# Performance work log

Hardware: AMD Instinct MI355X
Metric: run time of the kernel (lower is better)

The kernel has to match this reference:

```python
import jax, jax.numpy as jnp
from jax import lax
import numpy as np

D_MODEL = 1024
D_STATE = 128
D_CONV = 4
EXPAND = 2
HEADDIM = 64
CHUNK = 10
D_INNER = EXPAND * D_MODEL          # 2048
NHEADS = D_INNER // HEADDIM         # 32
CONV_DIM = D_INNER + 2 * D_STATE    # 2304
BATCH, SEQ = 2, 1000


def setup_inputs() -> dict:
    key = jax.random.key(0)
    ks = jax.random.split(key, 9)
    n = lambda k, shp, sc: jax.random.normal(k, shp, dtype=jnp.float32) * sc
    return {
        "x": n(ks[0], (BATCH, SEQ, D_MODEL), 1.0),
        "W_in": n(ks[1], (2 * D_INNER + 2 * D_STATE + NHEADS, D_MODEL), 0.02),
        "conv_w": n(ks[2], (CONV_DIM, D_CONV), 0.2),
        "conv_b": n(ks[3], (CONV_DIM,), 0.02),
        "dt_bias": n(ks[4], (NHEADS,), 0.5),
        "A_log": jnp.log(jnp.linspace(1.0, 16.0, NHEADS)).astype(jnp.float32),
        "D": n(ks[6], (NHEADS,), 1.0),
        "norm_w": jnp.ones((D_INNER,), jnp.float32),
        "W_out": n(ks[8], (D_MODEL, D_INNER), 0.02),
    }


def segsum(x):
    # x: (..., T) -> (..., T, T) with out[i,j] = sum_{k=j+1..i} x_k for i>=j else -inf
    cs = jnp.cumsum(x, axis=-1)
    seg = cs[..., :, None] - cs[..., None, :]
    T = x.shape[-1]
    mask = jnp.tril(jnp.ones((T, T), bool))
    return jnp.where(mask, seg, -jnp.inf)


def ssd(x, A, Bm, Cm, chunk):
    # x: (b,l,h,p)  A: (b,l,h)  Bm,Cm: (b,l,n)  (ngroups=1, group dim squeezed)
    b, l, h, p = x.shape
    n = Bm.shape[-1]
    c = l // chunk
    xr = x.reshape(b, c, chunk, h, p)
    Ar = A.reshape(b, c, chunk, h).transpose(0, 3, 1, 2)      # (b,h,c,s)
    Br = Bm.reshape(b, c, chunk, n)
    Cr = Cm.reshape(b, c, chunk, n)
    Acs = jnp.cumsum(Ar, axis=-1)                              # (b,h,c,s)
    L = jnp.exp(segsum(Ar))                                    # (b,h,c,s,s)
    # intra-chunk (diagonal blocks)
    Y_diag = jnp.einsum('bcln,bcsn,bhcls,bcshp->bclhp', Cr, Br, L, xr)
    # per-chunk end states
    decay_states = jnp.exp(Acs[..., -1:] - Acs)                # (b,h,c,s)
    states = jnp.einsum('bcln,bhcl,bclhp->bchpn', Br, decay_states, xr)
    states = jnp.concatenate([jnp.zeros((b, 1, h, p, n), x.dtype), states], axis=1)
    # inter-chunk recurrence (parallel form)
    chunk_sums = jnp.pad(Acs[..., -1], ((0, 0), (0, 0), (1, 0)))  # (b,h,c+1)
    decay_chunk = jnp.exp(segsum(chunk_sums))                    # (b,h,c+1,c+1)
    new_states = jnp.einsum('bhzc,bchpn->bzhpn', decay_chunk, states)
    prev_states = new_states[:, :-1]                             # (b,c,h,p,n)
    # state -> output contribution
    Y_off = jnp.einsum('bcln,bchpn,bhcl->bclhp', Cr, prev_states, jnp.exp(Acs))
    return (Y_diag + Y_off).reshape(b, l, h, p)


def reference(x, W_in, conv_w, conv_b, dt_bias, A_log, D, norm_w, W_out):
    b, l, _ = x.shape
    zxbcdt = x @ W_in.T                                          # (b,l,4384)
    z = zxbcdt[..., :D_INNER]
    xBC = zxbcdt[..., D_INNER:D_INNER + CONV_DIM]
    dt = zxbcdt[..., D_INNER + CONV_DIM:]
    dt = jax.nn.softplus(dt + dt_bias)                           # (b,l,h)
    # causal depthwise conv1d
    xc = jnp.pad(xBC, ((0, 0), (D_CONV - 1, 0), (0, 0)))
    conv = lax.conv_general_dilated(
        xc.transpose(0, 2, 1), conv_w[:, None, :], (1,), 'VALID',
        feature_group_count=CONV_DIM,
        dimension_numbers=('NCH', 'OIH', 'NCH'))
    xBC = jax.nn.silu(conv.transpose(0, 2, 1) + conv_b)          # (b,l,conv_dim)
    x_ssm = xBC[..., :D_INNER].reshape(b, l, NHEADS, HEADDIM)
    Bm = xBC[..., D_INNER:D_INNER + D_STATE]
    Cm = xBC[..., D_INNER + D_STATE:]
    A = -jnp.exp(A_log)                                          # (h,)
    y = ssd(x_ssm * dt[..., None], A * dt, Bm, Cm, CHUNK)
    y = y + x_ssm * D[None, None, :, None]
    y = y.reshape(b, l, D_INNER)
    # gated RMSNorm
    y = y * jax.nn.silu(z)
    y = y * lax.rsqrt(jnp.mean(y * y, axis=-1, keepdims=True) + 1e-5) * norm_w
    return y @ W_out.T
```

## Files before the change

### kernel.cpp

```cpp
#include <hip/hip_runtime.h>
#include <hip/hip_bf16.h>

#define BATCHN 2
#define SEQL 1000
#define DMODEL 1024
#define DSTATE 128
#define HEADDIM 64
#define DINNER 2048
#define NHEADS 32
#define CONVDIM 2304
#define NPROJ 4384
#define TOKENS 2000
#define MPAD 2048
#define NPAD1 4480
#define QC 64
#define NCH 16

typedef __bf16 bfx8 __attribute__((ext_vector_type(8)));
typedef float fx4 __attribute__((ext_vector_type(4)));
typedef unsigned short u16x8 __attribute__((ext_vector_type(8)));

__device__ __forceinline__ unsigned short f2bf(float f) {
    unsigned int u = __builtin_bit_cast(unsigned int, f);
    u += 0x7FFFu + ((u >> 16) & 1u);
    return (unsigned short)(u >> 16);
}
__device__ __forceinline__ float bf2f(unsigned short u) {
    return __builtin_bit_cast(float, ((unsigned int)u) << 16);
}

__device__ __forceinline__ void gload16(const void* g, void* l) {
    __builtin_amdgcn_global_load_lds(
        (const __attribute__((address_space(1))) void*)g,
        (__attribute__((address_space(3))) void*)l, 16, 0, 0);
}

__global__ __launch_bounds__(256) void k_f2bf_pad(const float* __restrict__ src,
                                                  unsigned short* __restrict__ dst,
                                                  int n4src, int n4dst) {
    int i = blockIdx.x * 256 + threadIdx.x;
    if (i >= n4dst) return;
    ushort4 o = {0, 0, 0, 0};
    if (i < n4src) {
        float4 v = ((const float4*)src)[i];
        o.x = f2bf(v.x); o.y = f2bf(v.y); o.z = f2bf(v.z); o.w = f2bf(v.w);
    }
    ((ushort4*)dst)[i] = o;
}

__global__ __launch_bounds__(256) void k_dt(const float* __restrict__ x,
                                            const float* __restrict__ win,
                                            const float* __restrict__ dt_bias,
                                            float* __restrict__ dtv) {
    __shared__ float sx[8][1024];
    int t = threadIdx.x;
    int tok0 = blockIdx.x * 8;
    for (int i = t; i < 8 * 256; i += 256) {
        int tok = i >> 8, k4 = i & 255;
        ((float4*)&sx[tok][0])[k4] = ((const float4*)(x + (size_t)(tok0 + tok) * DMODEL))[k4];
    }
    __syncthreads();
    int tl = t >> 5, h = t & 31;
    const float4* wr_ = (const float4*)(win + (size_t)(2 * DINNER + 2 * DSTATE + h) * DMODEL);
    const float4* xr = (const float4*)&sx[tl][0];
    float acc = 0.f;
    #pragma unroll 4
    for (int k = 0; k < 256; ++k) {
        float4 a = xr[k], b = wr_[k];
        acc += a.x * b.x + a.y * b.y + a.z * b.z + a.w * b.w;
    }
    float v = acc + dt_bias[h];
    dtv[(size_t)(tok0 + tl) * NHEADS + h] = fmaxf(v, 0.f) + log1pf(expf(-fabsf(v)));
}

__global__ __launch_bounds__(256) void k_gemm64(const unsigned short* __restrict__ A,
                                                const unsigned short* __restrict__ B,
                                                float* __restrict__ C,
                                                int Mstore, int N, int K,
                                                int kc, size_t pstride) {
    __shared__ __attribute__((aligned(16))) unsigned short As[2][2048];
    __shared__ __attribute__((aligned(16))) unsigned short Bs[2][4096];
    int t = threadIdx.x;
    int lane = t & 63, wave = t >> 6;
    int wr = wave >> 1, wc = wave & 1;
    int m0 = blockIdx.y * 64, n0 = blockIdx.x * 128;
    int k0 = blockIdx.z * kc;
    int swcol = (((t & 3) ^ ((t >> 3) & 3)) * 8);
    const unsigned short* Ag = A + (size_t)(m0 + (t >> 2)) * K + k0 + swcol;
    const unsigned short* Bg = B + (size_t)(n0 + (t >> 2)) * K + k0 + swcol;
    int fr = lane & 15, ks = lane >> 4;
    int sl = (ks ^ ((fr >> 1) & 3)) << 3;
    fx4 acc[2][4] = {};
    gload16(Ag, &As[0][t * 8]);
    gload16(Bg, &Bs[0][t * 8]);
    gload16(Bg + (size_t)64 * K, &Bs[0][2048 + t * 8]);
    __syncthreads();
    int cur = 0;
    for (int kk = 32; kk < kc; kk += 32) {
        gload16(Ag + kk, &As[cur ^ 1][t * 8]);
        gload16(Bg + kk, &Bs[cur ^ 1][t * 8]);
        gload16(Bg + (size_t)64 * K + kk, &Bs[cur ^ 1][2048 + t * 8]);
        bfx8 a[2], b[4];
        #pragma unroll
        for (int m = 0; m < 2; ++m)
            a[m] = *(const bfx8*)&As[cur][(wr * 32 + m * 16 + fr) * 32 + sl];
        #pragma unroll
        for (int n = 0; n < 4; ++n)
            b[n] = *(const bfx8*)&Bs[cur][(wc * 64 + n * 16 + fr) * 32 + sl];
        #pragma unroll
        for (int m = 0; m < 2; ++m)
            #pragma unroll
            for (int n = 0; n < 4; ++n)
                acc[m][n] = __builtin_amdgcn_mfma_f32_16x16x32_bf16(a[m], b[n], acc[m][n], 0, 0, 0);
        __syncthreads();
        cur ^= 1;
    }
    {
        bfx8 a[2], b[4];
        #pragma unroll
        for (int m = 0; m < 2; ++m)
            a[m] = *(const bfx8*)&As[cur][(wr * 32 + m * 16 + fr) * 32 + sl];
        #pragma unroll
        for (int n = 0; n < 4; ++n)
            b[n] = *(const bfx8*)&Bs[cur][(wc * 64 + n * 16 + fr) * 32 + sl];
        #pragma unroll
        for (int m = 0; m < 2; ++m)
            #pragma unroll
            for (int n = 0; n < 4; ++n)
                acc[m][n] = __builtin_amdgcn_mfma_f32_16x16x32_bf16(a[m], b[n], acc[m][n], 0, 0, 0);
    }
    float* Cz = C + (size_t)blockIdx.z * pstride;
    #pragma unroll
    for (int m = 0; m < 2; ++m) {
        int rbase = m0 + wr * 32 + m * 16 + (lane >> 4) * 4;
        #pragma unroll
        for (int i = 0; i < 4; ++i) {
            int r = rbase + i;
            if (r < Mstore) {
                #pragma unroll
                for (int n = 0; n < 4; ++n) {
                    int c = n0 + wc * 64 + n * 16 + fr;
                    if (c < N) Cz[(size_t)r * N + c] = acc[m][n][i];
                }
            }
        }
    }
}

__global__ __launch_bounds__(256) void k_red(const float* __restrict__ part,
                                             float* __restrict__ out, int n4, size_t pstride4) {
    int i = blockIdx.x * 256 + threadIdx.x;
    if (i >= n4) return;
    const float4* p = (const float4*)part;
    float4 v0 = p[i];
    float4 v1 = p[i + pstride4];
    float4 v2 = p[i + 2 * pstride4];
    float4 v3 = p[i + 3 * pstride4];
    float4 o;
    o.x = (v0.x + v1.x) + (v2.x + v3.x);
    o.y = (v0.y + v1.y) + (v2.y + v3.y);
    o.z = (v0.z + v1.z) + (v2.z + v3.z);
    o.w = (v0.w + v1.w) + (v2.w + v3.w);
    ((float4*)out)[i] = o;
}

__global__ __launch_bounds__(256) void k_conv4(const float* __restrict__ zx,
                                               const float* __restrict__ cw,
                                               const float* __restrict__ cb,
                                               float* __restrict__ xbc) {
    int idx = blockIdx.x * 256 + threadIdx.x;
    if (idx >= (TOKENS / 4) * CONVDIM) return;
    int tg = idx / CONVDIM;
    int col = idx - tg * CONVDIM;
    int b = tg / 250;
    int l0 = (tg - b * 250) * 4;
    float in[7];
    #pragma unroll
    for (int j = 0; j < 7; ++j) {
        int lj = l0 - 3 + j;
        in[j] = (lj >= 0) ? zx[(size_t)(b * SEQL + lj) * NPROJ + DINNER + col] : 0.f;
    }
    float w0 = cw[col * 4], w1 = cw[col * 4 + 1], w2 = cw[col * 4 + 2], w3 = cw[col * 4 + 3];
    float bb = cb[col];
    #pragma unroll
    for (int i = 0; i < 4; ++i) {
        float a = bb + w0 * in[i] + w1 * in[i + 1] + w2 * in[i + 2] + w3 * in[i + 3];
        xbc[(size_t)(b * SEQL + l0 + i) * CONVDIM + col] = a / (1.f + expf(-a));
    }
}

#define SCW 136
#define SWW 72
__global__ __launch_bounds__(256) void k_tile(const float* __restrict__ xbc,
                                              const float* __restrict__ dtv,
                                              const float* __restrict__ A_log,
                                              const float* __restrict__ Dp,
                                              float* __restrict__ ybuf,
                                              float* __restrict__ Sg,
                                              float* __restrict__ cumA) {
    __shared__ unsigned short sC[64 * SCW];
    __shared__ unsigned short sB[64 * SCW];
    __shared__ unsigned short sBdT[128 * SWW];
    __shared__ unsigned short sXdT[64 * SWW];
    __shared__ unsigned short sXr[64 * SWW];
    __shared__ float sAcs[64];
    __shared__ float sdt[64];
    int bid = blockIdx.x;
    int b = bid / (NHEADS * NCH);
    int r = bid % (NHEADS * NCH);
    int h = r / NCH, c = r % NCH;
    int t = threadIdx.x;
    int lane = t & 63, wave = t >> 6;
    if (t < 64) {
        int tok = c * QC + t;
        float d = (tok < SEQL) ? dtv[(size_t)(b * SEQL + tok) * NHEADS + h] : 0.f;
        float A = -expf(A_log[h]);
        float v = A * d;
        #pragma unroll
        for (int off = 1; off < 64; off <<= 1) {
            float u = __shfl_up(v, off, 64);
            if (lane >= off) v += u;
        }
        sdt[t] = d;
        sAcs[t] = v;
        cumA[(size_t)bid * 64 + t] = v;
    }
    __syncthreads();
    float Aend = sAcs[63];
    for (int i = t; i < 64 * 32; i += 256) {
        int l = i >> 5, n4 = (i & 31) * 4;
        int tok = c * QC + l;
        float4 cv = {0, 0, 0, 0}, bv = {0, 0, 0, 0};
        if (tok < SEQL) {
            const float* base = xbc + (size_t)(b * SEQL + tok) * CONVDIM;
            bv = *(const float4*)(base + DINNER + n4);
            cv = *(const float4*)(base + DINNER + DSTATE + n4);
        }
        float dec = expf(Aend - sAcs[l]);
        sC[l * SCW + n4 + 0] = f2bf(cv.x); sC[l * SCW + n4 + 1] = f2bf(cv.y);
        sC[l * SCW + n4 + 2] = f2bf(cv.z); sC[l * SCW + n4 + 3] = f2bf(cv.w);
        sB[l * SCW + n4 + 0] = f2bf(bv.x); sB[l * SCW + n4 + 1] = f2bf(bv.y);
        sB[l * SCW + n4 + 2] = f2bf(bv.z); sB[l * SCW + n4 + 3] = f2bf(bv.w);
        sBdT[(n4 + 0) * SWW + l] = f2bf(bv.x * dec);
        sBdT[(n4 + 1) * SWW + l] = f2bf(bv.y * dec);
        sBdT[(n4 + 2) * SWW + l] = f2bf(bv.z * dec);
        sBdT[(n4 + 3) * SWW + l] = f2bf(bv.w * dec);
    }
    for (int i = t; i < 64 * 16; i += 256) {
        int l = i >> 4, p4 = (i & 15) * 4;
        int tok = c * QC + l;
        float4 xv = {0, 0, 0, 0};
        if (tok < SEQL) xv = *(const float4*)(xbc + (size_t)(b * SEQL + tok) * CONVDIM + h * 64 + p4);
        float d = sdt[l];
        sXr[l * SWW + p4 + 0] = f2bf(xv.x); sXr[l * SWW + p4 + 1] = f2bf(xv.y);
        sXr[l * SWW + p4 + 2] = f2bf(xv.z); sXr[l * SWW + p4 + 3] = f2bf(xv.w);
        sXdT[(p4 + 0) * SWW + l] = f2bf(xv.x * d);
        sXdT[(p4 + 1) * SWW + l] = f2bf(xv.y * d);
        sXdT[(p4 + 2) * SWW + l] = f2bf(xv.z * d);
        sXdT[(p4 + 3) * SWW + l] = f2bf(xv.w * d);
    }
    __syncthreads();
    int fr = lane & 15, fk8 = (lane >> 4) * 8;
    int wr = wave >> 1, wc = wave & 1;
    fx4 g[2][2] = {};
    #pragma unroll
    for (int k = 0; k < 4; ++k) {
        bfx8 a0 = *(const bfx8*)&sC[(wr * 32 + fr) * SCW + k * 32 + fk8];
        bfx8 a1 = *(const bfx8*)&sC[(wr * 32 + 16 + fr) * SCW + k * 32 + fk8];
        bfx8 b0 = *(const bfx8*)&sB[(wc * 32 + fr) * SCW + k * 32 + fk8];
        bfx8 b1 = *(const bfx8*)&sB[(wc * 32 + 16 + fr) * SCW + k * 32 + fk8];
        g[0][0] = __builtin_amdgcn_mfma_f32_16x16x32_bf16(a0, b0, g[0][0], 0, 0, 0);
        g[0][1] = __builtin_amdgcn_mfma_f32_16x16x32_bf16(a0, b1, g[0][1], 0, 0, 0);
        g[1][0] = __builtin_amdgcn_mfma_f32_16x16x32_bf16(a1, b0, g[1][0], 0, 0, 0);
        g[1][1] = __builtin_amdgcn_mfma_f32_16x16x32_bf16(a1, b1, g[1][1], 0, 0, 0);
    }
    __syncthreads();
    int rb = wr * 32 + (lane >> 4) * 4;
    int cb = wc * 32 + fr;
    #pragma unroll
    for (int m = 0; m < 2; ++m)
        #pragma unroll
        for (int n = 0; n < 2; ++n)
            #pragma unroll
            for (int i = 0; i < 4; ++i) {
                int row = rb + m * 16 + i, col = cb + n * 16;
                float wv = (col <= row) ? g[m][n][i] * expf(sAcs[row] - sAcs[col]) : 0.f;
                sB[row * SWW + col] = f2bf(wv);
            }
    __syncthreads();
    fx4 yd[2][2] = {};
    fx4 sc[2][4] = {};
    #pragma unroll
    for (int k = 0; k < 2; ++k) {
        bfx8 aW0 = *(const bfx8*)&sB[(wr * 32 + fr) * SWW + k * 32 + fk8];
        bfx8 aW1 = *(const bfx8*)&sB[(wr * 32 + 16 + fr) * SWW + k * 32 + fk8];
        bfx8 bX0 = *(const bfx8*)&sXdT[(wc * 32 + fr) * SWW + k * 32 + fk8];
        bfx8 bX1 = *(const bfx8*)&sXdT[(wc * 32 + 16 + fr) * SWW + k * 32 + fk8];
        yd[0][0] = __builtin_amdgcn_mfma_f32_16x16x32_bf16(aW0, bX0, yd[0][0], 0, 0, 0);
        yd[0][1] = __builtin_amdgcn_mfma_f32_16x16x32_bf16(aW0, bX1, yd[0][1], 0, 0, 0);
        yd[1][0] = __builtin_amdgcn_mfma_f32_16x16x32_bf16(aW1, bX0, yd[1][0], 0, 0, 0);
        yd[1][1] = __builtin_amdgcn_mfma_f32_16x16x32_bf16(aW1, bX1, yd[1][1], 0, 0, 0);
        bfx8 aX0 = *(const bfx8*)&sXdT[(wr * 32 + fr) * SWW + k * 32 + fk8];
        bfx8 aX1 = *(const bfx8*)&sXdT[(wr * 32 + 16 + fr) * SWW + k * 32 + fk8];
        #pragma unroll
        for (int j = 0; j < 4; ++j) {
            bfx8 bB = *(const bfx8*)&sBdT[(wc * 64 + j * 16 + fr) * SWW + k * 32 + fk8];
            sc[0][j] = __builtin_amdgcn_mfma_f32_16x16x32_bf16(aX0, bB, sc[0][j], 0, 0, 0);
            sc[1][j] = __builtin_amdgcn_mfma_f32_16x16x32_bf16(aX1, bB, sc[1][j], 0, 0, 0);
        }
    }
    float Dh = Dp[h];
    #pragma unroll
    for (int m = 0; m < 2; ++m)
        #pragma unroll
        for (int i = 0; i < 4; ++i) {
            int row = rb + m * 16 + i;
            int tok = c * QC + row;
            if (tok < SEQL) {
                #pragma unroll
                for (int n = 0; n < 2; ++n) {
                    int col = cb + n * 16;
                    float xr = bf2f(sXr[row * SWW + col]);
                    ybuf[(size_t)(b * SEQL + tok) * DINNER + h * 64 + col] = yd[m][n][i] + Dh * xr;
                }
            }
        }
    #pragma unroll
    for (int m = 0; m < 2; ++m)
        #pragma unroll
        for (int i = 0; i < 4; ++i) {
            int p = rb + m * 16 + i;
            #pragma unroll
            for (int j = 0; j < 4; ++j) {
                int n = wc * 64 + j * 16 + fr;
                Sg[(size_t)bid * 8192 + p * 128 + n] = sc[m][j][i];
            }
        }
}

__global__ __launch_bounds__(256) void k_scan2v(float* __restrict__ Sg,
                                                const float* __restrict__ cumA) {
    int bid = blockIdx.x;
    int bh = bid >> 5, sub = bid & 31;
    int e = sub * 256 + threadIdx.x;
    __shared__ float sT[NCH];
    if (threadIdx.x < NCH)
        sT[threadIdx.x] = cumA[((size_t)(bh * NCH) + threadIdx.x) * 64 + 63];
    __syncthreads();
    float S = 0.f;
    size_t base = (size_t)bh * NCH * 8192 + e;
    for (int g = 0; g < NCH; ++g) {
        size_t off = base + (size_t)g * 8192;
        float sg = Sg[off];
        Sg[off] = S;
        S = expf(sT[g]) * S + sg;
    }
}

__global__ __launch_bounds__(256) void k_yoff(const float* __restrict__ xbc,
                                              const float* __restrict__ Sg,
                                              const float* __restrict__ cumA,
                                              float* __restrict__ ybuf) {
    int bid = blockIdx.x;
    int b = bid / (NHEADS * NCH);
    int r = bid % (NHEADS * NCH);
    int h = r / NCH, c = r % NCH;
    if (c == 0) return;
    __shared__ unsigned short sC[64 * SCW];
    __shared__ unsigned short sS[64 * SCW];
    __shared__ float sE[64];
    int t = threadIdx.x;
    int lane = t & 63, wave = t >> 6;
    if (t < 64) sE[t] = expf(cumA[(size_t)bid * 64 + t]);
    for (int i = t; i < 64 * 32; i += 256) {
        int l = i >> 5, n4 = (i & 31) * 4;
        int tok = c * QC + l;
        float4 cv = {0, 0, 0, 0};
        if (tok < SEQL)
            cv = *(const float4*)(xbc + (size_t)(b * SEQL + tok) * CONVDIM + DINNER + DSTATE + n4);
        sC[l * SCW + n4 + 0] = f2bf(cv.x); sC[l * SCW + n4 + 1] = f2bf(cv.y);
        sC[l * SCW + n4 + 2] = f2bf(cv.z); sC[l * SCW + n4 + 3] = f2bf(cv.w);
        float4 sv = *(const float4*)(Sg + (size_t)bid * 8192 + l * 128 + n4);
        sS[l * SCW + n4 + 0] = f2bf(sv.x); sS[l * SCW + n4 + 1] = f2bf(sv.y);
        sS[l * SCW + n4 + 2] = f2bf(sv.z); sS[l * SCW + n4 + 3] = f2bf(sv.w);
    }
    __syncthreads();
    int fr = lane & 15, fk8 = (lane >> 4) * 8;
    int wr = wave >> 1, wc = wave & 1;
    fx4 yo[2][2] = {};
    #pragma unroll
    for (int k = 0; k < 4; ++k) {
        bfx8 a0 = *(const bfx8*)&sC[(wr * 32 + fr) * SCW + k * 32 + fk8];
        bfx8 a1 = *(const bfx8*)&sC[(wr * 32 + 16 + fr) * SCW + k * 32 + fk8];
        bfx8 b0 = *(const bfx8*)&sS[(wc * 32 + fr) * SCW + k * 32 + fk8];
        bfx8 b1 = *(const bfx8*)&sS[(wc * 32 + 16 + fr) * SCW + k * 32 + fk8];
        yo[0][0] = __builtin_amdgcn_mfma_f32_16x16x32_bf16(a0, b0, yo[0][0], 0, 0, 0);
        yo[0][1] = __builtin_amdgcn_mfma_f32_16x16x32_bf16(a0, b1, yo[0][1], 0, 0, 0);
        yo[1][0] = __builtin_amdgcn_mfma_f32_16x16x32_bf16(a1, b0, yo[1][0], 0, 0, 0);
        yo[1][1] = __builtin_amdgcn_mfma_f32_16x16x32_bf16(a1, b1, yo[1][1], 0, 0, 0);
    }
    int rb = wr * 32 + (lane >> 4) * 4;
    int cb = wc * 32 + fr;
    #pragma unroll
    for (int m = 0; m < 2; ++m)
        #pragma unroll
        for (int i = 0; i < 4; ++i) {
            int row = rb + m * 16 + i;
            int tok = c * QC + row;
            if (tok < SEQL) {
                float e = sE[row];
                #pragma unroll
                for (int n = 0; n < 2; ++n) {
                    int col = cb + n * 16;
                    size_t off = (size_t)(b * SEQL + tok) * DINNER + h * 64 + col;
                    ybuf[off] += yo[m][n][i] * e;
                }
            }
        }
}

__global__ __launch_bounds__(256) void k_norm(const float* __restrict__ ybuf,
                                              const float* __restrict__ zx,
                                              const float* __restrict__ normw,
                                              unsigned short* __restrict__ ynb) {
    int row = blockIdx.x;
    int t = threadIdx.x;
    if (row >= TOKENS) {
        #pragma unroll
        for (int j = 0; j < 8; ++j) ynb[(size_t)row * DINNER + t + j * 256] = 0;
        return;
    }
    float v[8];
    float ss = 0.f;
    #pragma unroll
    for (int j = 0; j < 8; ++j) {
        int col = t + j * 256;
        float y = ybuf[(size_t)row * DINNER + col];
        float z = zx[(size_t)row * NPROJ + col];
        y *= z / (1.f + expf(-z));
        v[j] = y;
        ss += y * y;
    }
    #pragma unroll
    for (int off = 32; off > 0; off >>= 1) ss += __shfl_down(ss, off, 64);
    __shared__ float red[4];
    int lane = t & 63, wv = t >> 6;
    if (lane == 0) red[wv] = ss;
    __syncthreads();
    float tot = red[0] + red[1] + red[2] + red[3];
    float r = rsqrtf(tot * (1.f / DINNER) + 1e-5f);
    #pragma unroll
    for (int j = 0; j < 8; ++j) {
        int col = t + j * 256;
        ynb[(size_t)row * DINNER + col] = f2bf(v[j] * r * normw[col]);
    }
}

extern "C" void kernel_launch(void* const* d_in, const int* in_sizes, int n_in,
                              void* d_out, int out_size, void* d_ws, size_t ws_size,
                              hipStream_t stream) {
    const float* x       = (const float*)d_in[0];
    const float* W_in    = (const float*)d_in[1];
    const float* conv_w  = (const float*)d_in[2];
    const float* conv_b  = (const float*)d_in[3];
    const float* dt_bias = (const float*)d_in[4];
    const float* A_log   = (const float*)d_in[5];
    const float* Dp      = (const float*)d_in[6];
    const float* norm_w  = (const float*)d_in[7];
    const float* W_out   = (const float*)d_in[8];
    float* out = (float*)d_out;

    char* w = (char*)d_ws;
    auto alloc = [&](size_t bytes) {
        char* p = w;
        w += (bytes + 255) & ~(size_t)255;
        return p;
    };
    unsigned short* xb    = (unsigned short*)alloc((size_t)MPAD * DMODEL * 2);
    unsigned short* winb  = (unsigned short*)alloc((size_t)NPAD1 * DMODEL * 2);
    unsigned short* woutb = (unsigned short*)alloc((size_t)DMODEL * DINNER * 2);
    float* zx   = (float*)alloc((size_t)TOKENS * NPROJ * 4);
    float* xbc  = (float*)alloc((size_t)TOKENS * CONVDIM * 4);
    float* dtv  = (float*)alloc((size_t)TOKENS * NHEADS * 4);
    float* yb   = (float*)alloc((size_t)TOKENS * DINNER * 4);
    unsigned short* ynb = (unsigned short*)alloc((size_t)MPAD * DINNER * 2);
    float* Sg   = (float*)alloc((size_t)BATCHN * NHEADS * NCH * HEADDIM * DSTATE * 4);
    float* cumA = (float*)alloc((size_t)BATCHN * NHEADS * NCH * 64 * 4);

    int n4;
    n4 = MPAD * DMODEL / 4;
    k_f2bf_pad<<<(n4 + 255) / 256, 256, 0, stream>>>(x, xb, TOKENS * DMODEL / 4, n4);
    n4 = NPAD1 * DMODEL / 4;
    k_f2bf_pad<<<(n4 + 255) / 256, 256, 0, stream>>>(W_in, winb, NPROJ * DMODEL / 4, n4);
    n4 = DMODEL * DINNER / 4;
    k_f2bf_pad<<<(n4 + 255) / 256, 256, 0, stream>>>(W_out, woutb, n4, n4);
    k_dt<<<TOKENS / 8, 256, 0, stream>>>(x, W_in, dt_bias, dtv);
    dim3 g1(NPAD1 / 128, MPAD / 64, 1);
    k_gemm64<<<g1, 256, 0, stream>>>(xb, winb, zx, TOKENS, NPROJ, DMODEL, DMODEL, 0);
    k_conv4<<<(TOKENS / 4) * CONVDIM / 256, 256, 0, stream>>>(zx, conv_w, conv_b, xbc);
    k_tile<<<BATCHN * NHEADS * NCH, 256, 0, stream>>>(xbc, dtv, A_log, Dp, yb, Sg, cumA);
    k_scan2v<<<BATCHN * NHEADS * 32, 256, 0, stream>>>(Sg, cumA);
    k_yoff<<<BATCHN * NHEADS * NCH, 256, 0, stream>>>(xbc, Sg, cumA, yb);
    k_norm<<<MPAD, 256, 0, stream>>>(yb, zx, norm_w, ynb);
    size_t pstride = (size_t)MPAD * DMODEL;
    dim3 g2(DMODEL / 128, MPAD / 64, 4);
    k_gemm64<<<g2, 256, 0, stream>>>(ynb, woutb, zx, TOKENS, DMODEL, DINNER, DINNER / 4, pstride);
    n4 = TOKENS * DMODEL / 4;
    k_red<<<(n4 + 255) / 256, 256, 0, stream>>>(zx, out, n4, pstride / 4);
}
```

Before: 185.8 us.

## Triple-buffer GEMM with 64-wide K stages and halve out-proj split-K

The bf16 MFMA GEMM moves from a double-buffered 32-wide K step to a triple-buffered 64-wide K step. It uses an 8-slot XOR swizzle and explicit vmcnt waits, so global-to-LDS loads run two stages ahead of compute, with fewer barriers per K. The output projection's split-K factor drops from 4 to 2, and the reduction kernel now sums two partials instead of four. LDS use rises to about 72KB per block, which may reduce occupancy, and the out-proj grid now has half as many blocks.

```diff
diff --git a/kernel.cpp b/kernel.cpp
--- a/kernel.cpp
+++ b/kernel.cpp
@@ -35,6 +35,9 @@
         (__attribute__((address_space(3))) void*)l, 16, 0, 0);
 }
 
+#define VMCNT(n) asm volatile("s_waitcnt vmcnt(" #n ")" ::: "memory")
+#define BARF() do { __builtin_amdgcn_s_barrier(); asm volatile("" ::: "memory"); } while (0)
+
 __global__ __launch_bounds__(256) void k_f2bf_pad(const float* __restrict__ src,
                                                   unsigned short* __restrict__ dst,
                                                   int n4src, int n4dst) {
@@ -73,62 +76,74 @@
     dtv[(size_t)(tok0 + tl) * NHEADS + h] = fmaxf(v, 0.f) + log1pf(expf(-fabsf(v)));
 }
 
-__global__ __launch_bounds__(256) void k_gemm64(const unsigned short* __restrict__ A,
-                                                const unsigned short* __restrict__ B,
-                                                float* __restrict__ C,
-                                                int Mstore, int N, int K,
-                                                int kc, size_t pstride) {
-    __shared__ __attribute__((aligned(16))) unsigned short As[2][2048];
-    __shared__ __attribute__((aligned(16))) unsigned short Bs[2][4096];
+__global__ __launch_bounds__(256) void k_gemm64b(const unsigned short* __restrict__ A,
+                                                 const unsigned short* __restrict__ B,
+                                                 float* __restrict__ C,
+                                                 int Mstore, int N, int K,
+                                                 int kc, size_t pstride) {
+    __shared__ __attribute__((aligned(16))) unsigned short As[3][4096];
+    __shared__ __attribute__((aligned(16))) unsigned short Bs[3][8192];
     int t = threadIdx.x;
     int lane = t & 63, wave = t >> 6;
     int wr = wave >> 1, wc = wave & 1;
     int m0 = blockIdx.y * 64, n0 = blockIdx.x * 128;
     int k0 = blockIdx.z * kc;
-    int swcol = (((t & 3) ^ ((t >> 3) & 3)) * 8);
-    const unsigned short* Ag = A + (size_t)(m0 + (t >> 2)) * K + k0 + swcol;
-    const unsigned short* Bg = B + (size_t)(n0 + (t >> 2)) * K + k0 + swcol;
+    int nk = kc / 64;
+    int srow = t >> 3, sslot = t & 7;
+    int scol = ((sslot ^ (srow & 7)) * 8);
+    const unsigned short* Ag = A + (size_t)(m0 + srow) * K + k0 + scol;
+    const unsigned short* Bg = B + (size_t)(n0 + srow) * K + k0 + scol;
     int fr = lane & 15, ks = lane >> 4;
-    int sl = (ks ^ ((fr >> 1) & 3)) << 3;
     fx4 acc[2][4] = {};
-    gload16(Ag, &As[0][t * 8]);
-    gload16(Bg, &Bs[0][t * 8]);
-    gload16(Bg + (size_t)64 * K, &Bs[0][2048 + t * 8]);
-    __syncthreads();
-    int cur = 0;
-    for (int kk = 32; kk < kc; kk += 32) {
-        gload16(Ag + kk, &As[cur ^ 1][t * 8]);
-        gload16(Bg + kk, &Bs[cur ^ 1][t * 8]);
-        gload16(Bg + (size_t)64 * K + kk, &Bs[cur ^ 1][2048 + t * 8]);
-        bfx8 a[2], b[4];
-        #pragma unroll
-        for (int m = 0; m < 2; ++m)
-            a[m] = *(const bfx8*)&As[cur][(wr * 32 + m * 16 + fr) * 32 + sl];
-        #pragma unroll
-        for (int n = 0; n < 4; ++n)
-            b[n] = *(const bfx8*)&Bs[cur][(wc * 64 + n * 16 + fr) * 32 + sl];
-        #pragma unroll
-        for (int m = 0; m < 2; ++m)
-            #pragma unroll
-            for (int n = 0; n < 4; ++n)
-                acc[m][n] = __builtin_amdgcn_mfma_f32_16x16x32_bf16(a[m], b[n], acc[m][n], 0, 0, 0);
-        __syncthreads();
-        cur ^= 1;
-    }
-    {
-        bfx8 a[2], b[4];
-        #pragma unroll
-        for (int m = 0; m < 2; ++m)
-            a[m] = *(const bfx8*)&As[cur][(wr * 32 + m * 16 + fr) * 32 + sl];
-        #pragma unroll
-        for (int n = 0; n < 4; ++n)
-            b[n] = *(const bfx8*)&Bs[cur][(wc * 64 + n * 16 + fr) * 32 + sl];
-        #pragma unroll
-        for (int m = 0; m < 2; ++m)
-            #pragma unroll
-            for (int n = 0; n < 4; ++n)
-                acc[m][n] = __builtin_amdgcn_mfma_f32_16x16x32_bf16(a[m], b[n], acc[m][n], 0, 0, 0);
-    }
+
+#define STAGE64(bi, s) do {                                            \
+        int ko_ = (s) * 64;                                            \
+        gload16(Ag + ko_, &As[bi][t * 8]);                             \
+        gload16(Ag + (size_t)32 * K + ko_, &As[bi][2048 + t * 8]);     \
+        gload16(Bg + ko_, &Bs[bi][t * 8]);                             \
+        gload16(Bg + (size_t)32 * K + ko_, &Bs[bi][2048 + t * 8]);     \
+        gload16(Bg + (size_t)64 * K + ko_, &Bs[bi][4096 + t * 8]);     \
+        gload16(Bg + (size_t)96 * K + ko_, &Bs[bi][6144 + t * 8]);     \
+    } while (0)
+
+#define COMPUTE64(bi) do {                                             \
+        _Pragma("unroll")                                              \
+        for (int kh = 0; kh < 2; ++kh) {                               \
+            bfx8 a_[2], b_[4];                                         \
+            _Pragma("unroll")                                          \
+            for (int m = 0; m < 2; ++m) {                              \
+                int R = wr * 32 + m * 16 + fr;                         \
+                a_[m] = *(const bfx8*)&As[bi][R * 64 + (((kh * 4 + ks) ^ (R & 7)) << 3)]; \
+            }                                                          \
+            _Pragma("unroll")                                          \
+            for (int n = 0; n < 4; ++n) {                              \
+                int R = wc * 64 + n * 16 + fr;                         \
+                b_[n] = *(const bfx8*)&Bs[bi][R * 64 + (((kh * 4 + ks) ^ (R & 7)) << 3)]; \
+            }                                                          \
+            _Pragma("unroll")                                          \
+            for (int m = 0; m < 2; ++m)                                \
+                _Pragma("unroll")                                      \
+                for (int n = 0; n < 4; ++n)                            \
+                    acc[m][n] = __builtin_amdgcn_mfma_f32_16x16x32_bf16(a_[m], b_[n], acc[m][n], 0, 0, 0); \
+        }                                                              \
+    } while (0)
+
+    STAGE64(0, 0);
+    STAGE64(1, 1);
+    VMCNT(6);
+    BARF();
+    for (int k = 0; k + 2 < nk; ++k) {
+        STAGE64((k + 2) % 3, k + 2);
+        COMPUTE64(k % 3);
+        VMCNT(6);
+        BARF();
+    }
+    COMPUTE64((nk - 2) % 3);
+    VMCNT(0);
+    BARF();
+    COMPUTE64((nk - 1) % 3);
+#undef STAGE64
+#undef COMPUTE64
     float* Cz = C + (size_t)blockIdx.z * pstride;
     #pragma unroll
     for (int m = 0; m < 2; ++m) {
@@ -147,20 +162,18 @@
     }
 }
 
-__global__ __launch_bounds__(256) void k_red(const float* __restrict__ part,
-                                             float* __restrict__ out, int n4, size_t pstride4) {
+__global__ __launch_bounds__(256) void k_red2(const float* __restrict__ part,
+                                              float* __restrict__ out, int n4, size_t pstride4) {
     int i = blockIdx.x * 256 + threadIdx.x;
     if (i >= n4) return;
     const float4* p = (const float4*)part;
     float4 v0 = p[i];
     float4 v1 = p[i + pstride4];
-    float4 v2 = p[i + 2 * pstride4];
-    float4 v3 = p[i + 3 * pstride4];
     float4 o;
-    o.x = (v0.x + v1.x) + (v2.x + v3.x);
-    o.y = (v0.y + v1.y) + (v2.y + v3.y);
-    o.z = (v0.z + v1.z) + (v2.z + v3.z);
-    o.w = (v0.w + v1.w) + (v2.w + v3.w);
+    o.x = v0.x + v1.x;
+    o.y = v0.y + v1.y;
+    o.z = v0.z + v1.z;
+    o.w = v0.w + v1.w;
     ((float4*)out)[i] = o;
 }
 
@@ -496,15 +509,15 @@
     k_f2bf_pad<<<(n4 + 255) / 256, 256, 0, stream>>>(W_out, woutb, n4, n4);
     k_dt<<<TOKENS / 8, 256, 0, stream>>>(x, W_in, dt_bias, dtv);
     dim3 g1(NPAD1 / 128, MPAD / 64, 1);
-    k_gemm64<<<g1, 256, 0, stream>>>(xb, winb, zx, TOKENS, NPROJ, DMODEL, DMODEL, 0);
+    k_gemm64b<<<g1, 256, 0, stream>>>(xb, winb, zx, TOKENS, NPROJ, DMODEL, DMODEL, 0);
     k_conv4<<<(TOKENS / 4) * CONVDIM / 256, 256, 0, stream>>>(zx, conv_w, conv_b, xbc);
     k_tile<<<BATCHN * NHEADS * NCH, 256, 0, stream>>>(xbc, dtv, A_log, Dp, yb, Sg, cumA);
     k_scan2v<<<BATCHN * NHEADS * 32, 256, 0, stream>>>(Sg, cumA);
     k_yoff<<<BATCHN * NHEADS * NCH, 256, 0, stream>>>(xbc, Sg, cumA, yb);
     k_norm<<<MPAD, 256, 0, stream>>>(yb, zx, norm_w, ynb);
     size_t pstride = (size_t)MPAD * DMODEL;
-    dim3 g2(DMODEL / 128, MPAD / 64, 4);
-    k_gemm64<<<g2, 256, 0, stream>>>(ynb, woutb, zx, TOKENS, DMODEL, DINNER, DINNER / 4, pstride);
+    dim3 g2(DMODEL / 128, MPAD / 64, 2);
+    k_gemm64b<<<g2, 256, 0, stream>>>(ynb, woutb, zx, TOKENS, DMODEL, DINNER, DINNER / 2, pstride);
     n4 = TOKENS * DMODEL / 4;
-    k_red<<<(n4 + 255) / 256, 256, 0, stream>>>(zx, out, n4, pstride / 4);
-}
+    k_red2<<<(n4 + 255) / 256, 256, 0, stream>>>(zx, out, n4, pstride / 4);
+}
```

Result: no change. 189.5 us (+2.0%).
